# Performance work log

Hardware: AMD Instinct MI355X
Metric: run time of the kernel (lower is better)

## Reference

```python
import jax, jax.numpy as jnp
import numpy as np

DIM = 1024
HEADS = 16
HEAD_DIM = DIM // HEADS
FEAT = 256
B, N = 4, 4096


def setup_inputs() -> dict:
    key = jax.random.key(0)
    ks = jax.random.split(key, 10)
    s = 1.0 / np.sqrt(DIM)
    return {
        "x": jax.random.normal(ks[0], (B, N, DIM), jnp.float32),
        "Wq": jax.random.normal(ks[1], (DIM, DIM), jnp.float32) * s,
        "bq": jnp.zeros((DIM,), jnp.float32),
        "Wk": jax.random.normal(ks[2], (DIM, DIM), jnp.float32) * s,
        "bk": jnp.zeros((DIM,), jnp.float32),
        "Wv": jax.random.normal(ks[3], (DIM, DIM), jnp.float32) * s,
        "bv": jnp.zeros((DIM,), jnp.float32),
        "Wo": jax.random.normal(ks[4], (DIM, DIM), jnp.float32) * s,
        "bo": jnp.zeros((DIM,), jnp.float32),
        "random_features": jax.random.normal(ks[5], (HEAD_DIM, FEAT), jnp.float32) / np.sqrt(FEAT),
    }


def reference(x, Wq, bq, Wk, bk, Wv, bv, Wo, bo, random_features):
    Bsz, Nlen, C = x.shape
    # linear projections, reshape to (B, N, H, head_dim)
    q = (x @ Wq + bq).reshape(Bsz, Nlen, HEADS, HEAD_DIM)
    k = (x @ Wk + bk).reshape(Bsz, Nlen, HEADS, HEAD_DIM)
    v = (x @ Wv + bv).reshape(Bsz, Nlen, HEADS, HEAD_DIM)
    # positive feature map: elu(x)+1
    q = jax.nn.elu(q) + 1.0
    k = jax.nn.elu(k) + 1.0
    # random-feature projection (B, N, H, F)
    q = jnp.einsum('bnhd,df->bnhf', q, random_features)
    k = jnp.einsum('bnhd,df->bnhf', k, random_features)
    # kernelized linear attention (no normalization, non-causal as in source)
    kv = jnp.einsum('bnhf,bnhd->bhfd', k, v)          # (B, H, F, head_dim)
    out = jnp.einsum('bnhf,bhfd->bnhd', q, kv)        # (B, N, H, head_dim)
    out = out.reshape(Bsz, Nlen, C)
    return out @ Wo + bo
```

## Files before the change

### kernel.cpp

```cpp
#include <hip/hip_runtime.h>
#include <hip/hip_bf16.h>
#include <cstdint>
#include <cstddef>

using bf16 = __hip_bfloat16;
typedef __attribute__((ext_vector_type(8))) __bf16 bf16x8;
typedef __attribute__((ext_vector_type(4))) float f32x4;

typedef const __attribute__((address_space(1))) void CGV;
typedef __attribute__((address_space(3))) void LDSV;

__device__ __forceinline__ void gload_lds16(const void* g, void* l) {
    __builtin_amdgcn_global_load_lds((CGV*)g, (LDSV*)l, 16, 0, 0);
}

__device__ __forceinline__ float bits2f(unsigned short u) {
    return __uint_as_float(((unsigned)u) << 16);
}
__device__ __forceinline__ unsigned short f2bits(float f) {
    return __builtin_bit_cast(unsigned short, __float2bfloat16(f));
}

__global__ void cast_f32_bf16(const float4* __restrict__ in, ushort4* __restrict__ out, int n4) {
    int i = blockIdx.x * 256 + threadIdx.x;
    if (i < n4) {
        float4 f = in[i];
        ushort4 u;
        u.x = f2bits(f.x); u.y = f2bits(f.y); u.z = f2bits(f.z); u.w = f2bits(f.w);
        out[i] = u;
    }
}

__global__ void transpose_cast(const float* __restrict__ A, const float* __restrict__ B,
                               const float* __restrict__ C, bf16* __restrict__ Wt3) {
    const float* W = (blockIdx.z == 0) ? A : (blockIdx.z == 1) ? B : C;
    bf16* O = Wt3 + (size_t)blockIdx.z * (1024 * 1024);
    __shared__ float tile[32][33];
    int x = blockIdx.x * 32 + threadIdx.x;
    int y0 = blockIdx.y * 32;
    for (int i = threadIdx.y; i < 32; i += 8)
        tile[i][threadIdx.x] = W[(size_t)(y0 + i) * 1024 + x];
    __syncthreads();
    int xo = blockIdx.y * 32 + threadIdx.x;
    int yo = blockIdx.x * 32;
    for (int i = threadIdx.y; i < 32; i += 8)
        O[(size_t)(yo + i) * 1024 + xo] = __float2bfloat16(tile[threadIdx.x][i]);
}

__global__ void g_kernel(const float* __restrict__ RF, float* __restrict__ G) {
    int o = blockIdx.x * 256 + threadIdx.x;
    int i = o >> 6, j = o & 63;
    const float4* a = (const float4*)(RF + (size_t)i * 256);
    const float4* b = (const float4*)(RF + (size_t)j * 256);
    float s = 0.f;
    for (int f = 0; f < 64; f++) {
        float4 x = a[f], y = b[f];
        s += x.x * y.x + x.y * y.y + x.z * y.z + x.w * y.w;
    }
    G[o] = s;
}

__global__ __launch_bounds__(256, 2) void gemm_qkv(
    const bf16* __restrict__ X, const bf16* __restrict__ Wt3,
    const float* __restrict__ bq, const float* __restrict__ bk, const float* __restrict__ bv,
    bf16* __restrict__ Qo, bf16* __restrict__ Ko, bf16* __restrict__ Vo)
{
    __shared__ bf16 As[128 * 64];
    __shared__ bf16 Bs[128 * 64];
    const int z = blockIdx.z;
    const int n0 = blockIdx.x * 128;
    const int m0 = blockIdx.y * 128;
    const int tid = threadIdx.x;
    const int w = tid >> 6, lane = tid & 63;
    const int lr = lane >> 3, lc = lane & 7;
    const bf16* Wt = Wt3 + (size_t)z * (1024 * 1024);

    const bf16* ag = X  + (size_t)(m0 + w * 32 + lr) * 1024 + lc * 8;
    const bf16* bg = Wt + (size_t)(n0 + w * 32 + lr) * 1024 + lc * 8;
    bf16* al = As + (w * 32) * 64;
    bf16* bl = Bs + (w * 32) * 64;

    f32x4 acc[4][4];
#pragma unroll
    for (int i = 0; i < 4; i++)
#pragma unroll
        for (int j = 0; j < 4; j++) acc[i][j] = (f32x4){0.f, 0.f, 0.f, 0.f};

    const int lm = lane & 15, quad = lane >> 4;
    const bf16* Ab = As + ((w >> 1) * 64 + lm) * 64 + quad * 8;
    const bf16* Bb = Bs + ((w & 1) * 64 + lm) * 64 + quad * 8;

    for (int k0 = 0; k0 < 1024; k0 += 64) {
#pragma unroll
        for (int j = 0; j < 4; j++) {
            gload_lds16(ag + (size_t)j * 8 * 1024 + k0, al + j * 8 * 64);
            gload_lds16(bg + (size_t)j * 8 * 1024 + k0, bl + j * 8 * 64);
        }
        __syncthreads();
#pragma unroll
        for (int kk = 0; kk < 64; kk += 32) {
            bf16x8 a[4], b[4];
#pragma unroll
            for (int i = 0; i < 4; i++) a[i] = *(const bf16x8*)(Ab + i * 16 * 64 + kk);
#pragma unroll
            for (int i = 0; i < 4; i++) b[i] = *(const bf16x8*)(Bb + i * 16 * 64 + kk);
#pragma unroll
            for (int mi = 0; mi < 4; mi++)
#pragma unroll
                for (int ni = 0; ni < 4; ni++)
                    acc[mi][ni] = __builtin_amdgcn_mfma_f32_16x16x32_bf16(
                        a[mi], b[ni], acc[mi][ni], 0, 0, 0);
        }
        __syncthreads();
    }

    const float* bias = (z == 0) ? bq : (z == 1) ? bk : bv;
    bf16* Out = (z == 0) ? Qo : (z == 1) ? Ko : Vo;
    const int wr = (w >> 1) * 64, wc = (w & 1) * 64;
#pragma unroll
    for (int ni = 0; ni < 4; ni++) {
        int col = n0 + wc + ni * 16 + lm;
        float bs = bias[col];
#pragma unroll
        for (int mi = 0; mi < 4; mi++) {
            int row0 = m0 + wr + mi * 16 + quad * 4;
#pragma unroll
            for (int r = 0; r < 4; r++) {
                float v = acc[mi][ni][r] + bs;
                if (z != 2) v = (v > 0.f) ? (v + 1.f) : __expf(v);
                Out[(size_t)(row0 + r) * 1024 + col] = __float2bfloat16(v);
            }
        }
    }
}

__global__ __launch_bounds__(256) void s_kernel(const unsigned short* __restrict__ Kp,
                                                const unsigned short* __restrict__ Vp,
                                                float* __restrict__ Spart)
{
    int bh = blockIdx.x;
    int split = blockIdx.y;
    int b = bh >> 4, h = bh & 15;
    int t = threadIdx.x;
    int eb = (t >> 4) * 4, db = (t & 15) * 4;
    size_t rowbase = ((size_t)b * 4096 + (size_t)split * 512) * 1024 + h * 64;
    const unsigned short* kp = Kp + rowbase + eb;
    const unsigned short* vp = Vp + rowbase + db;
    float acc[4][4];
#pragma unroll
    for (int i = 0; i < 4; i++)
#pragma unroll
        for (int j = 0; j < 4; j++) acc[i][j] = 0.f;

    for (int n = 0; n < 512; n++) {
        ushort4 ku = *(const ushort4*)kp;
        ushort4 vu = *(const ushort4*)vp;
        float kf[4] = {bits2f(ku.x), bits2f(ku.y), bits2f(ku.z), bits2f(ku.w)};
        float vf[4] = {bits2f(vu.x), bits2f(vu.y), bits2f(vu.z), bits2f(vu.w)};
#pragma unroll
        for (int i = 0; i < 4; i++)
#pragma unroll
            for (int j = 0; j < 4; j++) acc[i][j] += kf[i] * vf[j];
        kp += 1024; vp += 1024;
    }
    float* sp = Spart + ((size_t)split * 64 + bh) * 4096;
#pragma unroll
    for (int i = 0; i < 4; i++)
#pragma unroll
        for (int j = 0; j < 4; j++) sp[(eb + i) * 64 + db + j] = acc[i][j];
}

__global__ void reduce_s(const float* __restrict__ Spart, float* __restrict__ S) {
    int bh = blockIdx.x, t = threadIdx.x;
    for (int v = 0; v < 4; v++) {
        int idx = v * 1024 + t * 4;
        float4 a = {0.f, 0.f, 0.f, 0.f};
        for (int s = 0; s < 8; s++) {
            float4 p = *(const float4*)&Spart[((size_t)s * 64 + bh) * 4096 + idx];
            a.x += p.x; a.y += p.y; a.z += p.z; a.w += p.w;
        }
        *(float4*)&S[(size_t)bh * 4096 + idx] = a;
    }
}

__global__ __launch_bounds__(256) void m_kernel(const float* __restrict__ S,
                                                const float* __restrict__ G,
                                                float* __restrict__ M)
{
    __shared__ float Sl[4096];
    int bh = blockIdx.x, t = threadIdx.x;
    for (int i = t; i < 4096; i += 256) Sl[i] = S[(size_t)bh * 4096 + i];
    __syncthreads();
    int e = t >> 2, d0 = (t & 3) * 16;
    float acc[16];
#pragma unroll
    for (int j = 0; j < 16; j++) acc[j] = 0.f;
    for (int ep = 0; ep < 64; ep++) {
        float g = G[e * 64 + ep];
#pragma unroll
        for (int j = 0; j < 16; j++) acc[j] += g * Sl[ep * 64 + d0 + j];
    }
#pragma unroll
    for (int j = 0; j < 16; j++) M[(size_t)bh * 4096 + e * 64 + d0 + j] = acc[j];
}

__global__ __launch_bounds__(256) void fold_kernel(const float* __restrict__ M,
                                                   const float* __restrict__ Wo,
                                                   bf16* __restrict__ Wo2t)
{
    int x = blockIdx.x;
    int b = x >> 6, h = (x >> 2) & 15, cb = x & 3;
    __shared__ float Ml[4096];
    int t = threadIdx.x;
    for (int i = t; i < 4096; i += 256) {
        int e = i >> 6, d = i & 63;
        Ml[d * 64 + e] = M[((size_t)b * 16 + h) * 4096 + i];
    }
    __syncthreads();
    int c = cb * 256 + t;
    float acc[64];
#pragma unroll
    for (int e = 0; e < 64; e++) acc[e] = 0.f;
    for (int d = 0; d < 64; d++) {
        float wo = Wo[(size_t)(h * 64 + d) * 1024 + c];
#pragma unroll
        for (int e = 0; e < 64; e++) acc[e] += Ml[d * 64 + e] * wo;
    }
    unsigned* outp = (unsigned*)(Wo2t + ((size_t)b * 1024 + c) * 1024 + h * 64);
#pragma unroll
    for (int e = 0; e < 64; e += 2) {
        unsigned lo = f2bits(acc[e]);
        unsigned hi = f2bits(acc[e + 1]);
        outp[e >> 1] = lo | (hi << 16);
    }
}

__global__ __launch_bounds__(256, 2) void gemm_out(
    const bf16* __restrict__ Qp, const bf16* __restrict__ Wo2t,
    const float* __restrict__ bo, float* __restrict__ Out)
{
    __shared__ bf16 As[128 * 64];
    __shared__ bf16 Bs[128 * 64];
    const int n0 = blockIdx.x * 128;
    const int m0 = blockIdx.y * 128;
    const int tid = threadIdx.x;
    const int w = tid >> 6, lane = tid & 63;
    const int lr = lane >> 3, lc = lane & 7;
    const bf16* Wt = Wo2t + (size_t)(m0 >> 12) * (1024 * 1024);

    const bf16* ag = Qp + (size_t)(m0 + w * 32 + lr) * 1024 + lc * 8;
    const bf16* bg = Wt + (size_t)(n0 + w * 32 + lr) * 1024 + lc * 8;
    bf16* al = As + (w * 32) * 64;
    bf16* bl = Bs + (w * 32) * 64;

    f32x4 acc[4][4];
#pragma unroll
    for (int i = 0; i < 4; i++)
#pragma unroll
        for (int j = 0; j < 4; j++) acc[i][j] = (f32x4){0.f, 0.f, 0.f, 0.f};

    const int lm = lane & 15, quad = lane >> 4;
    const bf16* Ab = As + ((w >> 1) * 64 + lm) * 64 + quad * 8;
    const bf16* Bb = Bs + ((w & 1) * 64 + lm) * 64 + quad * 8;

    for (int k0 = 0; k0 < 1024; k0 += 64) {
#pragma unroll
        for (int j = 0; j < 4; j++) {
            gload_lds16(ag + (size_t)j * 8 * 1024 + k0, al + j * 8 * 64);
            gload_lds16(bg + (size_t)j * 8 * 1024 + k0, bl + j * 8 * 64);
        }
        __syncthreads();
#pragma unroll
        for (int kk = 0; kk < 64; kk += 32) {
            bf16x8 a[4], b[4];
#pragma unroll
            for (int i = 0; i < 4; i++) a[i] = *(const bf16x8*)(Ab + i * 16 * 64 + kk);
#pragma unroll
            for (int i = 0; i < 4; i++) b[i] = *(const bf16x8*)(Bb + i * 16 * 64 + kk);
#pragma unroll
            for (int mi = 0; mi < 4; mi++)
#pragma unroll
                for (int ni = 0; ni < 4; ni++)
                    acc[mi][ni] = __builtin_amdgcn_mfma_f32_16x16x32_bf16(
                        a[mi], b[ni], acc[mi][ni], 0, 0, 0);
        }
        __syncthreads();
    }

    const int wr = (w >> 1) * 64, wc = (w & 1) * 64;
#pragma unroll
    for (int ni = 0; ni < 4; ni++) {
        int col = n0 + wc + ni * 16 + lm;
        float bs = bo[col];
#pragma unroll
        for (int mi = 0; mi < 4; mi++) {
            int row0 = m0 + wr + mi * 16 + quad * 4;
#pragma unroll
            for (int r = 0; r < 4; r++)
                Out[(size_t)(row0 + r) * 1024 + col] = acc[mi][ni][r] + bs;
        }
    }
}

extern "C" void kernel_launch(void* const* d_in, const int* in_sizes, int n_in,
                              void* d_out, int out_size, void* d_ws, size_t ws_size,
                              hipStream_t stream) {
    const float* x  = (const float*)d_in[0];
    const float* Wq = (const float*)d_in[1];
    const float* bq = (const float*)d_in[2];
    const float* Wk = (const float*)d_in[3];
    const float* bk = (const float*)d_in[4];
    const float* Wv = (const float*)d_in[5];
    const float* bv = (const float*)d_in[6];
    const float* Wo = (const float*)d_in[7];
    const float* bo = (const float*)d_in[8];
    const float* RF = (const float*)d_in[9];
    float* out = (float*)d_out;

    char* ws = (char*)d_ws;
    bf16*  Xb    = (bf16*) (ws);
    bf16*  Qp    = (bf16*) (ws + ((size_t)32  << 20));
    bf16*  Kp    = (bf16*) (ws + ((size_t)64  << 20));
    bf16*  Vp    = (bf16*) (ws + ((size_t)96  << 20));
    bf16*  Wt3   = (bf16*) (ws + ((size_t)128 << 20));
    bf16*  Wo2t  = (bf16*) (ws + ((size_t)134 << 20));
    float* Spart = (float*)(ws + ((size_t)142 << 20));
    float* S     = (float*)(ws + ((size_t)150 << 20));
    float* Mm    = (float*)(ws + ((size_t)151 << 20));
    float* G     = (float*)(ws + ((size_t)152 << 20));

    cast_f32_bf16<<<16384, 256, 0, stream>>>((const float4*)x, (ushort4*)Xb, 4194304);
    transpose_cast<<<dim3(32, 32, 3), dim3(32, 8), 0, stream>>>(Wq, Wk, Wv, Wt3);
    g_kernel<<<16, 256, 0, stream>>>(RF, G);
    gemm_qkv<<<dim3(8, 128, 3), 256, 0, stream>>>(Xb, Wt3, bq, bk, bv, Qp, Kp, Vp);
    s_kernel<<<dim3(64, 8), 256, 0, stream>>>((const unsigned short*)Kp,
                                              (const unsigned short*)Vp, Spart);
    reduce_s<<<64, 256, 0, stream>>>(Spart, S);
    m_kernel<<<64, 256, 0, stream>>>(S, G, Mm);
    fold_kernel<<<256, 256, 0, stream>>>(Mm, Wo, Wo2t);
    gemm_out<<<dim3(8, 128), 256, 0, stream>>>(Qp, Wo2t, bo, out);
}
```

Before: 471.7 us.

## Swizzle GEMM LDS tiles, remap blocks per XCD, head-major K/V with LDS-staged s_kernel

Both GEMMs now XOR-swizzle the 16-byte chunks they write into LDS and read back with the matching swizzle, to avoid LDS bank conflicts on the MFMA operand reads. Block indices are remapped so each XCD gets a contiguous band of M tiles, for better L2 reuse. The QKV GEMM writes K and V in a head-major (B,H,N,64) layout. s_kernel then stages contiguous 256-row K/V tiles into LDS with global_load_lds instead of doing strided global reads. The cost is more index arithmetic and scattered 2-byte stores in the QKV epilogue.

```diff
diff --git a/kernel.cpp b/kernel.cpp
--- a/kernel.cpp
+++ b/kernel.cpp
@@ -68,15 +68,18 @@
     __shared__ bf16 As[128 * 64];
     __shared__ bf16 Bs[128 * 64];
     const int z = blockIdx.z;
-    const int n0 = blockIdx.x * 128;
-    const int m0 = blockIdx.y * 128;
+    const int lid = blockIdx.x + (blockIdx.y << 3);
+    const int xcd = lid & 7, seq = lid >> 3;
+    const int m0 = (xcd * 16 + (seq >> 3)) * 128;
+    const int n0 = (seq & 7) * 128;
     const int tid = threadIdx.x;
     const int w = tid >> 6, lane = tid & 63;
     const int lr = lane >> 3, lc = lane & 7;
+    const int sc = lc ^ lr;
     const bf16* Wt = Wt3 + (size_t)z * (1024 * 1024);
 
-    const bf16* ag = X  + (size_t)(m0 + w * 32 + lr) * 1024 + lc * 8;
-    const bf16* bg = Wt + (size_t)(n0 + w * 32 + lr) * 1024 + lc * 8;
+    const bf16* ag = X  + (size_t)(m0 + w * 32 + lr) * 1024 + sc * 8;
+    const bf16* bg = Wt + (size_t)(n0 + w * 32 + lr) * 1024 + sc * 8;
     bf16* al = As + (w * 32) * 64;
     bf16* bl = Bs + (w * 32) * 64;
 
@@ -87,8 +90,10 @@
         for (int j = 0; j < 4; j++) acc[i][j] = (f32x4){0.f, 0.f, 0.f, 0.f};
 
     const int lm = lane & 15, quad = lane >> 4;
-    const bf16* Ab = As + ((w >> 1) * 64 + lm) * 64 + quad * 8;
-    const bf16* Bb = Bs + ((w & 1) * 64 + lm) * 64 + quad * 8;
+    const int x0 = (quad ^ (lm & 7)) * 8;
+    const int x1 = ((quad + 4) ^ (lm & 7)) * 8;
+    const bf16* Ab = As + ((w >> 1) * 64 + lm) * 64;
+    const bf16* Bb = Bs + ((w & 1) * 64 + lm) * 64;
 
     for (int k0 = 0; k0 < 1024; k0 += 64) {
 #pragma unroll
@@ -98,12 +103,13 @@
         }
         __syncthreads();
 #pragma unroll
-        for (int kk = 0; kk < 64; kk += 32) {
+        for (int kk = 0; kk < 2; kk++) {
+            const int xo = kk ? x1 : x0;
             bf16x8 a[4], b[4];
 #pragma unroll
-            for (int i = 0; i < 4; i++) a[i] = *(const bf16x8*)(Ab + i * 16 * 64 + kk);
-#pragma unroll
-            for (int i = 0; i < 4; i++) b[i] = *(const bf16x8*)(Bb + i * 16 * 64 + kk);
+            for (int i = 0; i < 4; i++) a[i] = *(const bf16x8*)(Ab + i * 16 * 64 + xo);
+#pragma unroll
+            for (int i = 0; i < 4; i++) b[i] = *(const bf16x8*)(Bb + i * 16 * 64 + xo);
 #pragma unroll
             for (int mi = 0; mi < 4; mi++)
 #pragma unroll
@@ -114,60 +120,96 @@
         __syncthreads();
     }
 
-    const float* bias = (z == 0) ? bq : (z == 1) ? bk : bv;
-    bf16* Out = (z == 0) ? Qo : (z == 1) ? Ko : Vo;
     const int wr = (w >> 1) * 64, wc = (w & 1) * 64;
-#pragma unroll
-    for (int ni = 0; ni < 4; ni++) {
-        int col = n0 + wc + ni * 16 + lm;
-        float bs = bias[col];
-#pragma unroll
-        for (int mi = 0; mi < 4; mi++) {
-            int row0 = m0 + wr + mi * 16 + quad * 4;
-#pragma unroll
-            for (int r = 0; r < 4; r++) {
-                float v = acc[mi][ni][r] + bs;
-                if (z != 2) v = (v > 0.f) ? (v + 1.f) : __expf(v);
-                Out[(size_t)(row0 + r) * 1024 + col] = __float2bfloat16(v);
+    if (z == 0) {
+#pragma unroll
+        for (int ni = 0; ni < 4; ni++) {
+            int col = n0 + wc + ni * 16 + lm;
+            float bs = bq[col];
+#pragma unroll
+            for (int mi = 0; mi < 4; mi++) {
+                int row0 = m0 + wr + mi * 16 + quad * 4;
+#pragma unroll
+                for (int r = 0; r < 4; r++) {
+                    float v = acc[mi][ni][r] + bs;
+                    v = (v > 0.f) ? (v + 1.f) : __expf(v);
+                    Qo[(size_t)(row0 + r) * 1024 + col] = __float2bfloat16(v);
+                }
             }
         }
-    }
-}
-
-__global__ __launch_bounds__(256) void s_kernel(const unsigned short* __restrict__ Kp,
-                                                const unsigned short* __restrict__ Vp,
-                                                float* __restrict__ Spart)
-{
-    int bh = blockIdx.x;
-    int split = blockIdx.y;
-    int b = bh >> 4, h = bh & 15;
-    int t = threadIdx.x;
-    int eb = (t >> 4) * 4, db = (t & 15) * 4;
-    size_t rowbase = ((size_t)b * 4096 + (size_t)split * 512) * 1024 + h * 64;
-    const unsigned short* kp = Kp + rowbase + eb;
-    const unsigned short* vp = Vp + rowbase + db;
+    } else {
+        const float* bias = (z == 1) ? bk : bv;
+        bf16* Out = (z == 1) ? Ko : Vo;
+#pragma unroll
+        for (int ni = 0; ni < 4; ni++) {
+            int col = n0 + wc + ni * 16 + lm;
+            float bs = bias[col];
+            int h = col >> 6, d = col & 63;
+#pragma unroll
+            for (int mi = 0; mi < 4; mi++) {
+                int row0 = m0 + wr + mi * 16 + quad * 4;
+#pragma unroll
+                for (int r = 0; r < 4; r++) {
+                    int row = row0 + r;
+                    int b = row >> 12, n = row & 4095;
+                    float v = acc[mi][ni][r] + bs;
+                    if (z == 1) v = (v > 0.f) ? (v + 1.f) : __expf(v);
+                    Out[(((size_t)(b * 16 + h) * 4096 + n) << 6) + d] = __float2bfloat16(v);
+                }
+            }
+        }
+    }
+}
+
+__global__ __launch_bounds__(256, 2) void s_kernel(const bf16* __restrict__ Kp,
+                                                   const bf16* __restrict__ Vp,
+                                                   float* __restrict__ Spart)
+{
+    __shared__ bf16 Ks[256 * 64];
+    __shared__ bf16 Vs[256 * 64];
+    const int bh = blockIdx.x, sp = blockIdx.y;
+    const int t = threadIdx.x;
+    const int w = t >> 6, lane = t & 63;
+    const int eb = (t >> 4) * 4, db = (t & 15) * 4;
+    const size_t base = ((size_t)bh * 4096 + sp * 512) * 64;
+
     float acc[4][4];
 #pragma unroll
     for (int i = 0; i < 4; i++)
 #pragma unroll
         for (int j = 0; j < 4; j++) acc[i][j] = 0.f;
 
-    for (int n = 0; n < 512; n++) {
-        ushort4 ku = *(const ushort4*)kp;
-        ushort4 vu = *(const ushort4*)vp;
-        float kf[4] = {bits2f(ku.x), bits2f(ku.y), bits2f(ku.z), bits2f(ku.w)};
-        float vf[4] = {bits2f(vu.x), bits2f(vu.y), bits2f(vu.z), bits2f(vu.w)};
-#pragma unroll
-        for (int i = 0; i < 4; i++)
-#pragma unroll
-            for (int j = 0; j < 4; j++) acc[i][j] += kf[i] * vf[j];
-        kp += 1024; vp += 1024;
-    }
-    float* sp = Spart + ((size_t)split * 64 + bh) * 4096;
+    const unsigned short* ks = (const unsigned short*)Ks;
+    const unsigned short* vs = (const unsigned short*)Vs;
+
+    for (int tile = 0; tile < 2; tile++) {
+        const bf16* kg = Kp + base + tile * (256 * 64) + (size_t)w * 4096 + lane * 8;
+        const bf16* vg = Vp + base + tile * (256 * 64) + (size_t)w * 4096 + lane * 8;
+#pragma unroll
+        for (int r = 0; r < 8; r++) {
+            gload_lds16(kg + r * 512, Ks + w * 4096 + r * 512);
+            gload_lds16(vg + r * 512, Vs + w * 4096 + r * 512);
+        }
+        __syncthreads();
+#pragma unroll 4
+        for (int n = 0; n < 256; n++) {
+            ushort4 ku = *(const ushort4*)(ks + n * 64 + eb);
+            ushort4 vu = *(const ushort4*)(vs + n * 64 + db);
+            float kf[4] = {bits2f(ku.x), bits2f(ku.y), bits2f(ku.z), bits2f(ku.w)};
+            float vf[4] = {bits2f(vu.x), bits2f(vu.y), bits2f(vu.z), bits2f(vu.w)};
+#pragma unroll
+            for (int i = 0; i < 4; i++)
+#pragma unroll
+                for (int j = 0; j < 4; j++) acc[i][j] += kf[i] * vf[j];
+        }
+        __syncthreads();
+    }
+
+    float* spb = Spart + ((size_t)sp * 64 + bh) * 4096;
 #pragma unroll
     for (int i = 0; i < 4; i++)
 #pragma unroll
-        for (int j = 0; j < 4; j++) sp[(eb + i) * 64 + db + j] = acc[i][j];
+        for (int j = 0; j < 4; j++) spb[(eb + i) * 64 + db + j] = acc[i][j];
 }
 
 __global__ void reduce_s(const float* __restrict__ Spart, float* __restrict__ S) {
@@ -175,8 +217,8 @@
     for (int v = 0; v < 4; v++) {
         int idx = v * 1024 + t * 4;
         float4 a = {0.f, 0.f, 0.f, 0.f};
-        for (int s = 0; s < 8; s++) {
-            float4 p = *(const float4*)&Spart[((size_t)s * 64 + bh) * 4096 + idx];
+        for (int s2 = 0; s2 < 8; s2++) {
+            float4 p = *(const float4*)&Spart[((size_t)s2 * 64 + bh) * 4096 + idx];
             a.x += p.x; a.y += p.y; a.z += p.z; a.w += p.w;
         }
         *(float4*)&S[(size_t)bh * 4096 + idx] = a;
@@ -241,15 +283,18 @@
 {
     __shared__ bf16 As[128 * 64];
     __shared__ bf16 Bs[128 * 64];
-    const int n0 = blockIdx.x * 128;
-    const int m0 = blockIdx.y * 128;
+    const int lid = blockIdx.x + (blockIdx.y << 3);
+    const int xcd = lid & 7, seq = lid >> 3;
+    const int m0 = (xcd * 16 + (seq >> 3)) * 128;
+    const int n0 = (seq & 7) * 128;
     const int tid = threadIdx.x;
     const int w = tid >> 6, lane = tid & 63;
     const int lr = lane >> 3, lc = lane & 7;
+    const int sc = lc ^ lr;
     const bf16* Wt = Wo2t + (size_t)(m0 >> 12) * (1024 * 1024);
 
-    const bf16* ag = Qp + (size_t)(m0 + w * 32 + lr) * 1024 + lc * 8;
-    const bf16* bg = Wt + (size_t)(n0 + w * 32 + lr) * 1024 + lc * 8;
+    const bf16* ag = Qp + (size_t)(m0 + w * 32 + lr) * 1024 + sc * 8;
+    const bf16* bg = Wt + (size_t)(n0 + w * 32 + lr) * 1024 + sc * 8;
     bf16* al = As + (w * 32) * 64;
     bf16* bl = Bs + (w * 32) * 64;
 
@@ -260,8 +305,10 @@
         for (int j = 0; j < 4; j++) acc[i][j] = (f32x4){0.f, 0.f, 0.f, 0.f};
 
     const int lm = lane & 15, quad = lane >> 4;
-    const bf16* Ab = As + ((w >> 1) * 64 + lm) * 64 + quad * 8;
-    const bf16* Bb = Bs + ((w & 1) * 64 + lm) * 64 + quad * 8;
+    const int x0 = (quad ^ (lm & 7)) * 8;
+    const int x1 = ((quad + 4) ^ (lm & 7)) * 8;
+    const bf16* Ab = As + ((w >> 1) * 64 + lm) * 64;
+    const bf16* Bb = Bs + ((w & 1) * 64 + lm) * 64;
 
     for (int k0 = 0; k0 < 1024; k0 += 64) {
 #pragma unroll
@@ -271,12 +318,13 @@
         }
         __syncthreads();
 #pragma unroll
-        for (int kk = 0; kk < 64; kk += 32) {
+        for (int kk = 0; kk < 2; kk++) {
+            const int xo = kk ? x1 : x0;
             bf16x8 a[4], b[4];
 #pragma unroll
-            for (int i = 0; i < 4; i++) a[i] = *(const bf16x8*)(Ab + i * 16 * 64 + kk);
-#pragma unroll
-            for (int i = 0; i < 4; i++) b[i] = *(const bf16x8*)(Bb + i * 16 * 64 + kk);
+            for (int i = 0; i < 4; i++) a[i] = *(const bf16x8*)(Ab + i * 16 * 64 + xo);
+#pragma unroll
+            for (int i = 0; i < 4; i++) b[i] = *(const bf16x8*)(Bb + i * 16 * 64 + xo);
 #pragma unroll
             for (int mi = 0; mi < 4; mi++)
 #pragma unroll
@@ -333,8 +381,7 @@
     transpose_cast<<<dim3(32, 32, 3), dim3(32, 8), 0, stream>>>(Wq, Wk, Wv, Wt3);
     g_kernel<<<16, 256, 0, stream>>>(RF, G);
     gemm_qkv<<<dim3(8, 128, 3), 256, 0, stream>>>(Xb, Wt3, bq, bk, bv, Qp, Kp, Vp);
-    s_kernel<<<dim3(64, 8), 256, 0, stream>>>((const unsigned short*)Kp,
-                                              (const unsigned short*)Vp, Spart);
+    s_kernel<<<dim3(64, 8), 256, 0, stream>>>(Kp, Vp, Spart);
     reduce_s<<<64, 256, 0, stream>>>(Spart, S);
     m_kernel<<<64, 256, 0, stream>>>(S, G, Mm);
     fold_kernel<<<256, 256, 0, stream>>>(Mm, Wo, Wo2t);
```

New measurement: 394.4 us. -16.4%, faster.
